# Optimization experiments

Measured on AMD Instinct MI355X. Metric: run time of the kernel, lower is better.

The kernel has to match this reference:

```python
import jax, jax.numpy as jnp
import numpy as np

NUM_EXPERTS = 64
TOP_K = 8
N_TOKENS = 131072  # batch*seq


def setup_inputs() -> dict:
    key = jax.random.key(0)
    k1, k2 = jax.random.split(key)
    top_scores = jax.random.uniform(k1, (N_TOKENS, TOP_K), dtype=jnp.float32)
    selected_experts_indices = jax.random.randint(
        k2, (N_TOKENS, TOP_K), 0, NUM_EXPERTS, dtype=jnp.int64
    )
    return {"top_scores": top_scores,
            "selected_experts_indices": selected_experts_indices}


def reference(top_scores, selected_experts_indices):
    flat_experts = selected_experts_indices.reshape(-1)          # (N*K,)
    # histogram of expert assignments (torch.histc with integer bins)
    num_tokens_per_expert = jnp.bincount(flat_experts, length=NUM_EXPERTS)
    # stable counting-sort permutation by expert id
    token_indices_experts_sorted = jnp.argsort(flat_experts, stable=True)
    top_scores_experts_sorted = top_scores.reshape(-1)[token_indices_experts_sorted]
    token_indices_experts_sorted = token_indices_experts_sorted // TOP_K
    return (top_scores_experts_sorted,
            token_indices_experts_sorted,
            num_tokens_per_expert)
```

## Files before the change

kernel.cpp:

```cpp
#include <hip/hip_runtime.h>

typedef unsigned int u32;
typedef unsigned long long u64;

#define NEXP    64
#define NB      256
#define EPB     4096
#define TPB     1024
#define WAVES   16
#define ROUNDS  4
#define LROWS   (NB / WAVES)
#define FLAG    0xC0000000u

__device__ __forceinline__ u32 ld_agent(const u32* p) {
    return __hip_atomic_load(p, __ATOMIC_RELAXED, __HIP_MEMORY_SCOPE_AGENT);
}

__global__ __launch_bounds__(TPB) void k_fused(
        const float* __restrict__ scores,
        const int*   __restrict__ experts,
        u32*         __restrict__ sshist,
        float* __restrict__ out_scores,
        float* __restrict__ out_idx,
        float* __restrict__ out_counts) {
    __shared__ u32 h[WAVES][NEXP];
    __shared__ u32 Pp[WAVES][NEXP], Tp[WAVES][NEXP];
    __shared__ u32 gBP[NEXP];
    __shared__ u32 lexcl[NEXP];
    __shared__ u64 pair[EPB];

    const int t = threadIdx.x, lane = t & 63, s = t >> 6, b = blockIdx.x;
    const int wbase = b * EPB + s * (ROUNDS * 64);

    int e[ROUNDS];
#pragma unroll
    for (int r = 0; r < ROUNDS; ++r) e[r] = experts[wbase + r * 64 + lane];
    u32 pv[LROWS];
#pragma unroll
    for (int k = 0; k < LROWS; ++k)
        pv[k] = ld_agent(&sshist[(s * LROWS + k) * NEXP + lane]);
    float sc[ROUNDS];
#pragma unroll
    for (int r = 0; r < ROUNDS; ++r) sc[r] = scores[wbase + r * 64 + lane];

    u64 m_lane[ROUNDS], mself[ROUNDS];
    u32 hc = 0;
#pragma unroll
    for (int r = 0; r < ROUNDS; ++r) {
        u64 bl[6];
#pragma unroll
        for (int bb = 0; bb < 6; ++bb) bl[bb] = __ballot((e[r] >> bb) & 1);
        u64 ml = ~0ull, ms = ~0ull;
#pragma unroll
        for (int bb = 0; bb < 6; ++bb) {
            ml &= ((lane >> bb) & 1)  ? bl[bb] : ~bl[bb];
            ms &= ((e[r] >> bb) & 1) ? bl[bb] : ~bl[bb];
        }
        hc += (u32)__popcll(ml);
        m_lane[r] = ml;
        mself[r]  = ms;
    }
    h[s][lane] = hc;
    __syncthreads();

    if (t < NEXP) {
        u32 H = 0;
#pragma unroll
        for (int w = 0; w < WAVES; ++w) H += h[w][t];
        __hip_atomic_store(&sshist[b * NEXP + t], H | FLAG,
                           __ATOMIC_RELAXED, __HIP_MEMORY_SCOPE_AGENT);
    }

    for (;;) {
        bool done = true;
#pragma unroll
        for (int k = 0; k < LROWS; ++k) {
            if ((pv[k] & FLAG) != FLAG) {
                pv[k] = ld_agent(&sshist[(s * LROWS + k) * NEXP + lane]);
                if ((pv[k] & FLAG) != FLAG) done = false;
            }
        }
        if (done) break;
    }

    u32 pall = 0, plt = 0;
#pragma unroll
    for (int k = 0; k < LROWS; ++k) {
        const int row = s * LROWS + k;
        const u32 x = pv[k] & 0xFFFFu;
        pall += x;
        if (row < b) plt += x;
    }
    Pp[s][lane] = plt;
    Tp[s][lane] = pall;
    __syncthreads();

    if (s == 0) {
        u32 P = 0, T = 0;
#pragma unroll
        for (int w = 0; w < WAVES; ++w) { P += Pp[w][lane]; T += Tp[w][lane]; }
        u32 x = T;
#pragma unroll
        for (int d = 1; d < 64; d <<= 1) {
            const u32 y = __shfl_up(x, d);
            if (lane >= d) x += y;
        }
        gBP[lane] = (x - T) + P;
        if (b == 0) out_counts[lane] = (float)T;
    } else if (s == 1) {
        u32 H = 0;
#pragma unroll
        for (int w = 0; w < WAVES; ++w) H += h[w][lane];
        u32 z = H;
#pragma unroll
        for (int d = 1; d < 64; d <<= 1) {
            const u32 y = __shfl_up(z, d);
            if (lane >= d) z += y;
        }
        lexcl[lane] = z - H;
    }
    __syncthreads();

    u32 cur = lexcl[lane];
    for (int w = 0; w < s; ++w) cur += h[w][lane];

    const u64 lt = (1ull << lane) - 1ull;
#pragma unroll
    for (int r = 0; r < ROUNDS; ++r) {
        const u32 slot = (u32)__shfl((int)cur, e[r])
                       + (u32)__popcll(mself[r] & lt);
        const u32 gi = (u32)(wbase + r * 64 + lane);
        pair[slot] = ((u64)__float_as_uint(sc[r]) << 32)
                   | ((gi >> 3) << 6) | (u32)e[r];
        cur += (u32)__popcll(m_lane[r]);
    }
    __syncthreads();

#pragma unroll
    for (int r = 0; r < ROUNDS; ++r) {
        const int j = r * TPB + t;
        const u64 v = pair[j];
        const u32 lo = (u32)v;
        const u32 ee = lo & 63u;
        const u32 dst = gBP[ee] - lexcl[ee] + (u32)j;
        out_scores[dst] = __uint_as_float((u32)(v >> 32));
        out_idx[dst]    = (float)(lo >> 6);
    }
}

extern "C" void kernel_launch(void* const* d_in, const int* in_sizes, int n_in,
                              void* d_out, int out_size, void* d_ws, size_t ws_size,
                              hipStream_t stream) {
    const float* top_scores = (const float*)d_in[0];
    const int*   experts    = (const int*)d_in[1];

    const int M = in_sizes[0];

    u32* sshist = (u32*)d_ws;

    float* out = (float*)d_out;

    k_fused<<<NB, TPB, 0, stream>>>(top_scores, experts, sshist,
                                    out, out + M, out + 2 * (size_t)M);
}
```

Measured before the change: 13.12 us.

## Double block count, replace flag spin with batched load and fallback, shuffle offsets

Uses twice as many blocks, each handling half as many elements, and asks for higher occupancy in launch bounds. The upfront prefetch plus retry loop over the cross-block histogram is replaced by batched agent-scope loads of every row, with a per-row spin used only if any flag is still missing. Ranks and counts are computed early to free registers, and the global offset per expert is now fetched by a wave shuffle instead of two LDS reads. More blocks shorten per-block work but double the histogram rows each block must read. The spin wait also assumes all 512 blocks are resident at once, which risks deadlock if they are not.

```diff
diff --git a/kernel.cpp b/kernel.cpp
--- a/kernel.cpp
+++ b/kernel.cpp
@@ -4,11 +4,11 @@
 typedef unsigned long long u64;
 
 #define NEXP    64
-#define NB      256
-#define EPB     4096
+#define NB      512
+#define EPB     2048
 #define TPB     1024
 #define WAVES   16
-#define ROUNDS  4
+#define ROUNDS  2
 #define LROWS   (NB / WAVES)
 #define FLAG    0xC0000000u
 
@@ -16,7 +16,7 @@
     return __hip_atomic_load(p, __ATOMIC_RELAXED, __HIP_MEMORY_SCOPE_AGENT);
 }
 
-__global__ __launch_bounds__(TPB) void k_fused(
+__global__ __launch_bounds__(TPB, 8) void k_fused(
         const float* __restrict__ scores,
         const int*   __restrict__ experts,
         u32*         __restrict__ sshist,
@@ -35,15 +35,12 @@
     int e[ROUNDS];
 #pragma unroll
     for (int r = 0; r < ROUNDS; ++r) e[r] = experts[wbase + r * 64 + lane];
-    u32 pv[LROWS];
-#pragma unroll
-    for (int k = 0; k < LROWS; ++k)
-        pv[k] = ld_agent(&sshist[(s * LROWS + k) * NEXP + lane]);
     float sc[ROUNDS];
 #pragma unroll
     for (int r = 0; r < ROUNDS; ++r) sc[r] = scores[wbase + r * 64 + lane];
 
-    u64 m_lane[ROUNDS], mself[ROUNDS];
+    const u64 lt = (1ull << lane) - 1ull;
+    u32 rank[ROUNDS], hcnt[ROUNDS];
     u32 hc = 0;
 #pragma unroll
     for (int r = 0; r < ROUNDS; ++r) {
@@ -56,9 +53,9 @@
             ml &= ((lane >> bb) & 1)  ? bl[bb] : ~bl[bb];
             ms &= ((e[r] >> bb) & 1) ? bl[bb] : ~bl[bb];
         }
-        hc += (u32)__popcll(ml);
-        m_lane[r] = ml;
-        mself[r]  = ms;
+        rank[r] = (u32)__popcll(ms & lt);
+        hcnt[r] = (u32)__popcll(ml);
+        hc += hcnt[r];
     }
     h[s][lane] = hc;
     __syncthreads();
@@ -71,25 +68,34 @@
                            __ATOMIC_RELAXED, __HIP_MEMORY_SCOPE_AGENT);
     }
 
-    for (;;) {
-        bool done = true;
+    u32 pall = 0, plt = 0;
+    bool bad = false;
 #pragma unroll
+    for (int kk = 0; kk < LROWS; kk += 8) {
+        u32 x8[8];
+#pragma unroll
+        for (int j = 0; j < 8; ++j)
+            x8[j] = ld_agent(&sshist[(s * LROWS + kk + j) * NEXP + lane]);
+#pragma unroll
+        for (int j = 0; j < 8; ++j) {
+            const int row = s * LROWS + kk + j;
+            bad |= ((x8[j] & FLAG) != FLAG);
+            const u32 x = x8[j] & 0xFFFFu;
+            pall += x;
+            if (row < b) plt += x;
+        }
+    }
+    if (__any((int)bad)) {
+        pall = 0; plt = 0;
         for (int k = 0; k < LROWS; ++k) {
-            if ((pv[k] & FLAG) != FLAG) {
-                pv[k] = ld_agent(&sshist[(s * LROWS + k) * NEXP + lane]);
-                if ((pv[k] & FLAG) != FLAG) done = false;
-            }
+            const int row = s * LROWS + k;
+            u32 x = ld_agent(&sshist[row * NEXP + lane]);
+            while ((x & FLAG) != FLAG)
+                x = ld_agent(&sshist[row * NEXP + lane]);
+            x &= 0xFFFFu;
+            pall += x;
+            if (row < b) plt += x;
         }
-        if (done) break;
-    }
-
-    u32 pall = 0, plt = 0;
-#pragma unroll
-    for (int k = 0; k < LROWS; ++k) {
-        const int row = s * LROWS + k;
-        const u32 x = pv[k] & 0xFFFFu;
-        pall += x;
-        if (row < b) plt += x;
     }
     Pp[s][lane] = plt;
     Tp[s][lane] = pall;
@@ -121,18 +127,18 @@
     }
     __syncthreads();
 
-    u32 cur = lexcl[lane];
+    const u32 lex = lexcl[lane];
+    u32 cur = lex;
     for (int w = 0; w < s; ++w) cur += h[w][lane];
+    const u32 gadj = gBP[lane] - lex;
 
-    const u64 lt = (1ull << lane) - 1ull;
 #pragma unroll
     for (int r = 0; r < ROUNDS; ++r) {
-        const u32 slot = (u32)__shfl((int)cur, e[r])
-                       + (u32)__popcll(mself[r] & lt);
+        const u32 slot = (u32)__shfl((int)cur, e[r]) + rank[r];
         const u32 gi = (u32)(wbase + r * 64 + lane);
         pair[slot] = ((u64)__float_as_uint(sc[r]) << 32)
                    | ((gi >> 3) << 6) | (u32)e[r];
-        cur += (u32)__popcll(m_lane[r]);
+        cur += hcnt[r];
     }
     __syncthreads();
 
@@ -141,8 +147,7 @@
         const int j = r * TPB + t;
         const u64 v = pair[j];
         const u32 lo = (u32)v;
-        const u32 ee = lo & 63u;
-        const u32 dst = gBP[ee] - lexcl[ee] + (u32)j;
+        const u32 dst = (u32)__shfl((int)gadj, (int)(lo & 63u)) + (u32)j;
         out_scores[dst] = __uint_as_float((u32)(v >> 32));
         out_idx[dst]    = (float)(lo >> 6);
     }
```

Result: slower. 18.06 us (+37.7%).
